# Optimization experiments

Hardware: AMD Instinct MI355X
Metric: run time of the kernel (lower is better)

## Reference

```python
import jax, jax.numpy as jnp
import numpy as np

N = 50000
E = 800000
NUM_GRAPHS = 128
X_IN, HID, EDGE_DIM = 64, 64, 16


def setup_inputs() -> dict:
    key = jax.random.key(0)
    ks = jax.random.split(key, 9)
    s = 0.05
    inp = {
        'x': jax.random.normal(ks[0], (N, X_IN), jnp.float32),
        'edge_index': jax.random.randint(ks[1], (2, E), 0, N, dtype=jnp.int32),
        'edge_attr': jax.random.normal(ks[2], (E, EDGE_DIM), jnp.float32),
        'batch': jnp.sort(jax.random.randint(ks[3], (N,), 0, NUM_GRAPHS, dtype=jnp.int32)),
        'w_fc1': jax.random.normal(ks[4], (EDGE_DIM, 1), jnp.float32) * s,
        'b_fc1': jnp.zeros((1,), jnp.float32),
    }
    dims = [(X_IN, HID), (HID, HID * 2), (HID * 2, HID)]
    for i, (din, dout) in enumerate(dims):
        k1, k2, k3 = jax.random.split(ks[5 + i], 3)
        inp[f'w1_{i}'] = jax.random.normal(k1, (din, dout), jnp.float32) * s
        inp[f'b1_{i}'] = jnp.zeros((dout,), jnp.float32)
        inp[f'w2_{i}'] = jax.random.normal(k2, (din, dout), jnp.float32) * s
        inp[f'w3_{i}'] = jax.random.normal(k3, (din, dout), jnp.float32) * s
        inp[f'b3_{i}'] = jnp.zeros((dout,), jnp.float32)
    return inp


def leconv(x, src, dst, ew, w1, b1, w2, w3, b3):
    # PyG LEConv: out_i = lin3(x_i) + sum_{j->i} e_ji * (lin1(x_j) - lin2(x_i))
    a = x @ w1 + b1          # lin1 (bias=True)   [N, out]
    b = x @ w2               # lin2 (bias=False)  [N, out]
    msg = ew[:, None] * (a[src] - b[dst])          # [E, out]
    agg = jax.ops.segment_sum(msg, dst, num_segments=N)
    return agg + x @ w3 + b3  # lin3 (bias=True)


def reference(x, edge_index, edge_attr, batch,
              w_fc1, b_fc1,
              w1_0, b1_0, w2_0, w3_0, b3_0,
              w1_1, b1_1, w2_1, w3_1, b3_1,
              w1_2, b1_2, w2_2, w3_2, b3_2):
    src, dst = edge_index[0], edge_index[1]
    ew = (edge_attr @ w_fc1 + b_fc1)[:, 0]         # fc1(edge_attr).squeeze(-1) -> [E]
    h = jax.nn.elu(leconv(x, src, dst, ew, w1_0, b1_0, w2_0, w3_0, b3_0))
    h = jax.nn.elu(leconv(h, src, dst, ew, w1_1, b1_1, w2_1, w3_1, b3_1))
    h = jax.nn.elu(leconv(h, src, dst, ew, w1_2, b1_2, w2_2, w3_2, b3_2))
    # global max pool over nodes of each graph -> [NUM_GRAPHS, HID]
    return jax.ops.segment_max(h, batch, num_segments=NUM_GRAPHS)
```

## Files before the change

### kernel.cpp

```cpp
#include <hip/hip_runtime.h>
#include <math.h>

#define N_NODES 50000
#define N_EDGES 800000
#define NUM_GRAPHS_ 128
#define SCAN_NB 98
#define NPASS 8
#define NODES_PER_PASS 6250
#define HCHUNKS 128
#define EDGES_PER_CHUNK 6250
#define HWORDS 12500

typedef unsigned short u16;
typedef unsigned int u32;
typedef __attribute__((ext_vector_type(8))) short bf16x8;
typedef __attribute__((ext_vector_type(4))) float f32x4;

__device__ __forceinline__ float elu_f(float v) {
    return v > 0.f ? v : (__expf(v) - 1.f);
}
__device__ __forceinline__ u16 f2bf(float f) {
    u32 u = __float_as_uint(f);
    u += 0x7FFFu + ((u >> 16) & 1u);
    return (u16)(u >> 16);
}
__device__ __forceinline__ float bf2f(u16 h) {
    return __uint_as_float(((u32)h) << 16);
}
__device__ __forceinline__ void bfpair(u32 v, float& lo, float& hi) {
    lo = __uint_as_float(v << 16);
    hi = __uint_as_float(v & 0xFFFF0000u);
}
__device__ __forceinline__ u32 packbf(float lo, float hi) {
    return (u32)f2bf(lo) | ((u32)f2bf(hi) << 16);
}

__global__ void conv_x_kernel(const float* __restrict__ x, u16* __restrict__ xb) {
    int g = blockIdx.x * blockDim.x + threadIdx.x;
    float4 v = ((const float4*)x)[g];
    uint2 o;
    o.x = packbf(v.x, v.y);
    o.y = packbf(v.z, v.w);
    ((uint2*)xb)[g] = o;
}

__global__ void ew_kernel(const float* __restrict__ edge_attr,
                          const float* __restrict__ w_fc1,
                          const float* __restrict__ b_fc1,
                          const int* __restrict__ edge_index,
                          float* __restrict__ ew,
                          u16* __restrict__ dst16) {
    int e = blockIdx.x * blockDim.x + threadIdx.x;
    if (e >= N_EDGES) return;
    const float4* ea = (const float4*)(edge_attr + (size_t)e * 16);
    const float4* wf = (const float4*)w_fc1;
    float acc = b_fc1[0];
#pragma unroll
    for (int i = 0; i < 4; i++) {
        float4 a = ea[i], w = wf[i];
        acc += a.x * w.x + a.y * w.y + a.z * w.z + a.w * w.w;
    }
    ew[e] = acc;
    dst16[e] = (u16)edge_index[N_EDGES + e];
}

__global__ __launch_bounds__(256) void deg_hist_kernel(const u16* __restrict__ dst16,
                                                       u32* __restrict__ partial) {
    __shared__ u32 bins[HWORDS];
    const int c = blockIdx.x >> 1;
    const int p = blockIdx.x & 1;
    const int t = threadIdx.x;
    for (int i = t; i < HWORDS; i += 256) bins[i] = 0;
    __syncthreads();
    const int base = c * EDGES_PER_CHUNK;
    const int nlo = p * 25000;
    for (int i = t; i < EDGES_PER_CHUNK; i += 256) {
        const int b = (int)dst16[base + i] - nlo;
        if ((unsigned)b < 25000u)
            atomicAdd(&bins[b >> 1], 1u << ((b & 1) * 16));
    }
    __syncthreads();
    u32* outp = partial + (size_t)blockIdx.x * HWORDS;
    for (int i = t; i < HWORDS; i += 256) outp[i] = bins[i];
}

__global__ __launch_bounds__(256) void scan_chunks_kernel(const u32* __restrict__ partial,
                                                          u32* __restrict__ prefpack,
                                                          u32* __restrict__ degpack) {
    const int g = blockIdx.x * 256 + threadIdx.x;
    if (g >= 25000) return;
    const int p = (g >= HWORDS) ? 1 : 0;
    const int wh = g - p * HWORDS;
    u32 runlo = 0, runhi = 0;
    for (int c = 0; c < HCHUNKS; c++) {
        prefpack[(size_t)c * 25000 + g] = runlo | (runhi << 16);
        u32 v = partial[(size_t)((c << 1) + p) * HWORDS + wh];
        runlo += v & 0xFFFFu;
        runhi += v >> 16;
    }
    degpack[g] = runlo | (runhi << 16);
}

__global__ __launch_bounds__(256) void scan1_kernel(const u32* __restrict__ degpack,
                                                    int* __restrict__ rowptr,
                                                    int* __restrict__ blk_sums) {
    __shared__ int sh[256];
    const int t = threadIdx.x;
    const int base = blockIdx.x * 512;
    const int i0 = base + 2 * t, i1 = i0 + 1;
    int d0 = 0, d1 = 0;
    if (i0 < N_NODES) {
        u32 v = degpack[i0 >> 1];
        d0 = (int)(v & 0xFFFFu);
        d1 = (int)(v >> 16);
    }
    const int pair = d0 + d1;
    int v = pair;
    sh[t] = v;
    __syncthreads();
#pragma unroll
    for (int off = 1; off < 256; off <<= 1) {
        int add = (t >= off) ? sh[t - off] : 0;
        __syncthreads();
        v += add;
        sh[t] = v;
        __syncthreads();
    }
    const int excl = v - pair;
    if (i0 < N_NODES) rowptr[i0] = excl;
    if (i1 < N_NODES) rowptr[i1] = excl + d0;
    if (t == 255) blk_sums[blockIdx.x] = v;
}

__global__ __launch_bounds__(128) void scan2_kernel(const int* __restrict__ blk_sums,
                                                    int* __restrict__ blk_offs,
                                                    int* __restrict__ rowptr) {
    __shared__ int sh[128];
    const int t = threadIdx.x;
    const int orig = (t < SCAN_NB) ? blk_sums[t] : 0;
    int v = orig;
    sh[t] = v;
    __syncthreads();
#pragma unroll
    for (int off = 1; off < 128; off <<= 1) {
        int add = (t >= off) ? sh[t - off] : 0;
        __syncthreads();
        v += add;
        sh[t] = v;
        __syncthreads();
    }
    if (t < SCAN_NB) blk_offs[t] = v - orig;
    if (t == 127) rowptr[N_NODES] = v;
}

__global__ void scan3_kernel(int* __restrict__ rowptr,
                             const int* __restrict__ blk_offs) {
    int i = blockIdx.x * blockDim.x + threadIdx.x;
    if (i >= N_NODES) return;
    rowptr[i] += blk_offs[i >> 9];
}

__global__ __launch_bounds__(256) void place_kernel(const int* __restrict__ edge_index,
                                                    const float* __restrict__ ew,
                                                    const u16* __restrict__ dst16,
                                                    const int* __restrict__ rowptr,
                                                    const u32* __restrict__ prefpack,
                                                    int2* __restrict__ csr) {
    __shared__ int lcur[NODES_PER_PASS];
    const int pass = blockIdx.x & (NPASS - 1);
    const int c = blockIdx.x >> 3;
    const int lo = pass * NODES_PER_PASS;
    const int t = threadIdx.x;
    for (int i = t; i < NODES_PER_PASS; i += 256) lcur[i] = 0;
    __syncthreads();
    const int base = c * EDGES_PER_CHUNK;
    for (int i = t; i < EDGES_PER_CHUNK; i += 256) {
        const int e = base + i;
        const int d = (int)dst16[e];
        const int dl = d - lo;
        if ((unsigned)dl < (unsigned)NODES_PER_PASS) {
            u32 pw = prefpack[(size_t)c * 25000 + (d >> 1)];
            int pref = (int)((pw >> ((d & 1) * 16)) & 0xFFFFu);
            int lpos = atomicAdd(&lcur[dl], 1);
            int2 ent;
            ent.x = edge_index[e];
            ent.y = __float_as_int(ew[e]);
            csr[rowptr[d] + pref + lpos] = ent;
        }
    }
}

template <int DIN, bool WRITE_C>
__global__ __launch_bounds__(256) void gather_kernel(
    const u16* __restrict__ xb, const int* __restrict__ rowptr,
    const int2* __restrict__ csr, u16* __restrict__ sb,
    u16* __restrict__ chb, float* __restrict__ c) {
    constexpr int CG = DIN / 4;
    constexpr int EG = 64 / CG;
    const int gid = blockIdx.x * 256 + threadIdx.x;
    const int node = gid >> 6;
    if (node >= N_NODES) return;
    const int lane = threadIdx.x & 63;
    const int cg = lane & (CG - 1);
    const int eg = lane / CG;
    const int beg = rowptr[node];
    const int end = rowptr[node + 1];
    const uint2* x2 = (const uint2*)xb;

    float a0 = 0.f, a1 = 0.f, a2 = 0.f, a3 = 0.f;
    float b0 = 0.f, b1 = 0.f, b2 = 0.f, b3 = 0.f;
    float wsum = 0.f;

    int p = beg + eg;
    for (; p + EG < end; p += 2 * EG) {
        int2 e0 = csr[p];
        int2 e1 = csr[p + EG];
        float w0 = __int_as_float(e0.y);
        float w1 = __int_as_float(e1.y);
        uint2 v0 = x2[(size_t)e0.x * CG + cg];
        uint2 v1 = x2[(size_t)e1.x * CG + cg];
        float f0, f1, f2, f3, g0, g1, g2, g3;
        bfpair(v0.x, f0, f1); bfpair(v0.y, f2, f3);
        bfpair(v1.x, g0, g1); bfpair(v1.y, g2, g3);
        a0 += w0 * f0; a1 += w0 * f1; a2 += w0 * f2; a3 += w0 * f3;
        b0 += w1 * g0; b1 += w1 * g1; b2 += w1 * g2; b3 += w1 * g3;
        wsum += w0 + w1;
    }
    if (p < end) {
        int2 e0 = csr[p];
        float w0 = __int_as_float(e0.y);
        uint2 v0 = x2[(size_t)e0.x * CG + cg];
        float f0, f1, f2, f3;
        bfpair(v0.x, f0, f1); bfpair(v0.y, f2, f3);
        a0 += w0 * f0; a1 += w0 * f1; a2 += w0 * f2; a3 += w0 * f3;
        wsum += w0;
    }
    a0 += b0; a1 += b1; a2 += b2; a3 += b3;

#pragma unroll
    for (int off = 32; off >= CG; off >>= 1) {
        a0 += __shfl_xor(a0, off);
        a1 += __shfl_xor(a1, off);
        a2 += __shfl_xor(a2, off);
        a3 += __shfl_xor(a3, off);
        wsum += __shfl_xor(wsum, off);
    }

    if (lane < CG) {
        uint2 so;
        so.x = packbf(a0, a1);
        so.y = packbf(a2, a3);
        ((uint2*)sb)[(size_t)node * CG + cg] = so;
        const float cn = WRITE_C ? wsum : c[node];
        uint2 hv = x2[(size_t)node * CG + cg];
        float h0, h1, h2, h3;
        bfpair(hv.x, h0, h1); bfpair(hv.y, h2, h3);
        uint2 co;
        co.x = packbf(cn * h0, cn * h1);
        co.y = packbf(cn * h2, cn * h3);
        ((uint2*)chb)[(size_t)node * CG + cg] = co;
    }
    if (WRITE_C && lane == 0) c[node] = wsum;
}

__global__ void pack_w_kernel(const float* __restrict__ w3_0, const float* __restrict__ w1_0, const float* __restrict__ w2_0,
                              const float* __restrict__ w3_1, const float* __restrict__ w1_1, const float* __restrict__ w2_1,
                              const float* __restrict__ w3_2, const float* __restrict__ w1_2, const float* __restrict__ w2_2,
                              u16* __restrict__ bp0, u16* __restrict__ bp1, u16* __restrict__ bp2) {
    int t = blockIdx.x * blockDim.x + threadIdx.x;
    if (t >= 7680) return;
    u16 buf[8];
    if (t < 4608) {
        int DIN, DOUT, lid;
        const float *w3, *w1, *w2;
        u16* bp;
        if (t < 1536) { DIN = 64; DOUT = 64;  lid = t;        w3 = w3_0; w1 = w1_0; w2 = w2_0; bp = bp0; }
        else          { DIN = 64; DOUT = 128; lid = t - 1536; w3 = w3_1; w1 = w1_1; w2 = w2_1; bp = bp1; }
        const int NT = DOUT / 16;
        const int lane = lid & 63;
        const int fragid = lid >> 6;
        const int chunk = fragid / NT;
        const int ntile = fragid % NT;
        const int n = ntile * 16 + (lane & 15);
        const int kbase = chunk * 32 + (lane >> 4) * 8;
#pragma unroll
        for (int j = 0; j < 8; j++) {
            int k = kbase + j;
            int region = k / DIN;
            int kk = k - region * DIN;
            float v = (region == 0) ? w3[kk * DOUT + n]
                    : (region == 1) ? w1[kk * DOUT + n]
                                    : -w2[kk * DOUT + n];
            buf[j] = f2bf(v);
        }
        *(bf16x8*)(bp + ((size_t)lid << 3)) = *(bf16x8*)buf;
    } else {
        const int lid = t - 4608;
        const int NT = 12;
        const int lane = lid & 63;
        const int fragid = lid >> 6;
        const int chunk = fragid / NT;
        const int ntile = fragid % NT;
        const int n = ntile * 16 + (lane & 15);
        const int kbase = chunk * 32 + (lane >> 4) * 8;
#pragma unroll
        for (int j = 0; j < 8; j++) {
            int k = kbase + j;
            float v = (n < 64)  ? w3_2[k * 64 + n]
                    : (n < 128) ? -w2_2[k * 64 + (n - 64)]
                                : w1_2[k * 64 + (n - 128)];
            buf[j] = f2bf(v);
        }
        *(bf16x8*)(bp2 + ((size_t)lid << 3)) = *(bf16x8*)buf;
    }
}

template <int DIN, int DOUT>
__global__ __launch_bounds__(256) void gemm_mfma(
    const u16* __restrict__ hb, const u16* __restrict__ sb,
    const u16* __restrict__ chb, const u16* __restrict__ Bp,
    const float* __restrict__ cvec, const float* __restrict__ bias1,
    const float* __restrict__ bias3, u16* __restrict__ outp) {
    constexpr int CH = DIN / 32;
    constexpr int CHUNKS = 3 * CH;
    constexpr int NT = DOUT / 16;
    const int tid = threadIdx.x;
    const int wv = tid >> 6;
    const int lane = tid & 63;
    const int l15 = lane & 15;
    const int q = lane >> 4;
    const int mhalf = wv & 1;
    const int nhalf = wv >> 1;
    const int row_base = blockIdx.x * 64 + mhalf * 32;
    const int nt0 = blockIdx.y * 4 + nhalf * 2;

    const int r0 = min(row_base + l15, N_NODES - 1);
    const int r1 = min(row_base + 16 + l15, N_NODES - 1);
    const int qo = q * 8;

    f32x4 acc00 = {0.f, 0.f, 0.f, 0.f};
    f32x4 acc01 = {0.f, 0.f, 0.f, 0.f};
    f32x4 acc10 = {0.f, 0.f, 0.f, 0.f};
    f32x4 acc11 = {0.f, 0.f, 0.f, 0.f};

#pragma unroll
    for (int chunk = 0; chunk < CHUNKS; chunk++) {
        const int region = chunk / CH;
        const int koff = (chunk - region * CH) * 32 + qo;
        const u16* A = (region == 0) ? hb : (region == 1) ? sb : chb;
        bf16x8 a0 = *(const bf16x8*)(A + (size_t)r0 * DIN + koff);
        bf16x8 a1 = *(const bf16x8*)(A + (size_t)r1 * DIN + koff);
        const u16* bp = Bp + (((size_t)(chunk * NT + nt0) * 64 + lane) << 3);
        bf16x8 bf0 = *(const bf16x8*)bp;
        bf16x8 bf1 = *(const bf16x8*)(bp + 64 * 8);
        acc00 = __builtin_amdgcn_mfma_f32_16x16x32_bf16(a0, bf0, acc00, 0, 0, 0);
        acc01 = __builtin_amdgcn_mfma_f32_16x16x32_bf16(a0, bf1, acc01, 0, 0, 0);
        acc10 = __builtin_amdgcn_mfma_f32_16x16x32_bf16(a1, bf0, acc10, 0, 0, 0);
        acc11 = __builtin_amdgcn_mfma_f32_16x16x32_bf16(a1, bf1, acc11, 0, 0, 0);
    }

#pragma unroll
    for (int ni = 0; ni < 2; ni++) {
        const int col = (nt0 + ni) * 16 + l15;
        const float B3 = bias3[col];
        const float B1 = bias1[col];
        const f32x4 am0 = ni ? acc01 : acc00;
        const f32x4 am1 = ni ? acc11 : acc10;
#pragma unroll
        for (int mi = 0; mi < 2; mi++) {
            const f32x4 av = mi ? am1 : am0;
#pragma unroll
            for (int reg = 0; reg < 4; reg++) {
                const int row = row_base + mi * 16 + q * 4 + reg;
                if (row < N_NODES) {
                    const float cv = cvec[row];
                    const float val = av[reg] + B3 + cv * B1;
                    outp[(size_t)row * DOUT + col] = f2bf(elu_f(val));
                }
            }
        }
    }
}

__global__ __launch_bounds__(256) void gemm_l1_fused(
    const u16* __restrict__ hb, const u16* __restrict__ sb,
    const u16* __restrict__ chb, const u16* __restrict__ Bp1,
    const u16* __restrict__ Bp2, const float* __restrict__ cvec,
    const float* __restrict__ bias1, const float* __restrict__ bias3,
    u16* __restrict__ zuy) {
    __shared__ u16 ht[64][136];
    const int tid = threadIdx.x;
    const int wv = tid >> 6;
    const int lane = tid & 63;
    const int l15 = lane & 15;
    const int q = lane >> 4;
    const int mhalf = wv & 1;
    const int nhalf = wv >> 1;
    const int row_base = blockIdx.x * 64 + mhalf * 32;
    const int r0 = min(row_base + l15, N_NODES - 1);
    const int r1 = min(row_base + 16 + l15, N_NODES - 1);
    const int qo = q * 8;

    {
        const int nt0 = nhalf * 4;
        f32x4 acc[2][4] = {};
#pragma unroll
        for (int chunk = 0; chunk < 6; chunk++) {
            const int region = chunk / 2;
            const int koff = (chunk - region * 2) * 32 + qo;
            const u16* A = (region == 0) ? hb : (region == 1) ? sb : chb;
            bf16x8 a0 = *(const bf16x8*)(A + (size_t)r0 * 64 + koff);
            bf16x8 a1 = *(const bf16x8*)(A + (size_t)r1 * 64 + koff);
#pragma unroll
            for (int ni = 0; ni < 4; ni++) {
                bf16x8 bf = *(const bf16x8*)(Bp1 + (((size_t)(chunk * 8 + nt0 + ni) * 64 + lane) << 3));
                acc[0][ni] = __builtin_amdgcn_mfma_f32_16x16x32_bf16(a0, bf, acc[0][ni], 0, 0, 0);
                acc[1][ni] = __builtin_amdgcn_mfma_f32_16x16x32_bf16(a1, bf, acc[1][ni], 0, 0, 0);
            }
        }
#pragma unroll
        for (int ni = 0; ni < 4; ni++) {
            const int col = (nt0 + ni) * 16 + l15;
            const float B3 = bias3[col];
            const float B1 = bias1[col];
#pragma unroll
            for (int mi = 0; mi < 2; mi++) {
#pragma unroll
                for (int reg = 0; reg < 4; reg++) {
                    const int lrow = mhalf * 32 + mi * 16 + q * 4 + reg;
                    const int grow = blockIdx.x * 64 + lrow;
                    const float cv = cvec[min(grow, N_NODES - 1)];
                    ht[lrow][col] = f2bf(elu_f(acc[mi][ni][reg] + B3 + cv * B1));
                }
            }
        }
    }
    __syncthreads();

    {
        const int nt2 = nhalf * 6;
        f32x4 acc[2][6] = {};
#pragma unroll
        for (int chunk = 0; chunk < 4; chunk++) {
            const int koff = chunk * 32 + qo;
            bf16x8 a0 = *(const bf16x8*)(&ht[mhalf * 32 + l15][koff]);
            bf16x8 a1 = *(const bf16x8*)(&ht[mhalf * 32 + 16 + l15][koff]);
#pragma unroll
            for (int ni = 0; ni < 6; ni++) {
                bf16x8 bf = *(const bf16x8*)(Bp2 + (((size_t)(chunk * 12 + nt2 + ni) * 64 + lane) << 3));
                acc[0][ni] = __builtin_amdgcn_mfma_f32_16x16x32_bf16(a0, bf, acc[0][ni], 0, 0, 0);
                acc[1][ni] = __builtin_amdgcn_mfma_f32_16x16x32_bf16(a1, bf, acc[1][ni], 0, 0, 0);
            }
        }
#pragma unroll
        for (int ni = 0; ni < 6; ni++) {
            const int col = (nt2 + ni) * 16 + l15;
#pragma unroll
            for (int mi = 0; mi < 2; mi++) {
#pragma unroll
                for (int reg = 0; reg < 4; reg++) {
                    const int row = row_base + mi * 16 + q * 4 + reg;
                    if (row < N_NODES)
                        zuy[(size_t)row * 192 + col] = f2bf(acc[mi][ni][reg]);
                }
            }
        }
    }
}

__global__ __launch_bounds__(256) void gather2_kernel(
    const u16* __restrict__ zuy, const int* __restrict__ rowptr,
    const int2* __restrict__ csr, const float* __restrict__ c,
    const float* __restrict__ bias1, const float* __restrict__ bias3,
    u16* __restrict__ h3) {
    constexpr int CG = 16, EG = 4;
    const int gid = blockIdx.x * 256 + threadIdx.x;
    const int node = gid >> 6;
    if (node >= N_NODES) return;
    const int lane = threadIdx.x & 63;
    const int cg = lane & (CG - 1);
    const int eg = lane >> 4;
    const int beg = rowptr[node];
    const int end = rowptr[node + 1];

    float a0 = 0.f, a1 = 0.f, a2 = 0.f, a3 = 0.f;
    float b0 = 0.f, b1 = 0.f, b2 = 0.f, b3 = 0.f;

    int p = beg + eg;
    for (; p + EG < end; p += 2 * EG) {
        int2 e0 = csr[p];
        int2 e1 = csr[p + EG];
        float w0 = __int_as_float(e0.y);
        float w1 = __int_as_float(e1.y);
        uint2 v0 = ((const uint2*)(zuy + (size_t)e0.x * 192 + 128))[cg];
        uint2 v1 = ((const uint2*)(zuy + (size_t)e1.x * 192 + 128))[cg];
        float f0, f1, f2, f3, g0, g1, g2, g3;
        bfpair(v0.x, f0, f1); bfpair(v0.y, f2, f3);
        bfpair(v1.x, g0, g1); bfpair(v1.y, g2, g3);
        a0 += w0 * f0; a1 += w0 * f1; a2 += w0 * f2; a3 += w0 * f3;
        b0 += w1 * g0; b1 += w1 * g1; b2 += w1 * g2; b3 += w1 * g3;
    }
    if (p < end) {
        int2 e0 = csr[p];
        float w0 = __int_as_float(e0.y);
        uint2 v0 = ((const uint2*)(zuy + (size_t)e0.x * 192 + 128))[cg];
        float f0, f1, f2, f3;
        bfpair(v0.x, f0, f1); bfpair(v0.y, f2, f3);
        a0 += w0 * f0; a1 += w0 * f1; a2 += w0 * f2; a3 += w0 * f3;
    }
    a0 += b0; a1 += b1; a2 += b2; a3 += b3;

#pragma unroll
    for (int off = 32; off >= CG; off >>= 1) {
        a0 += __shfl_xor(a0, off);
        a1 += __shfl_xor(a1, off);
        a2 += __shfl_xor(a2, off);
        a3 += __shfl_xor(a3, off);
    }

    if (lane < CG) {
        const float cn = c[node];
        const u16* zr = zuy + (size_t)node * 192;
        uint2 zv = ((const uint2*)zr)[cg];
        uint2 uv = ((const uint2*)(zr + 64))[cg];
        float z0, z1, z2, z3, u0, u1, u2, u3;
        bfpair(zv.x, z0, z1); bfpair(zv.y, z2, z3);
        bfpair(uv.x, u0, u1); bfpair(uv.y, u2, u3);
        const float4 b3v = *(const float4*)(bias3 + cg * 4);
        const float4 b1v = *(const float4*)(bias1 + cg * 4);
        float o0 = elu_f(z0 + cn * u0 + a0 + b3v.x + cn * b1v.x);
        float o1 = elu_f(z1 + cn * u1 + a1 + b3v.y + cn * b1v.y);
        float o2 = elu_f(z2 + cn * u2 + a2 + b3v.z + cn * b1v.z);
        float o3 = elu_f(z3 + cn * u3 + a3 + b3v.w + cn * b1v.w);
        uint2 o;
        o.x = packbf(o0, o1);
        o.y = packbf(o2, o3);
        ((uint2*)h3)[(size_t)node * CG + cg] = o;
    }
}

__global__ void pool_kernel(const u16* __restrict__ h,
                            const int* __restrict__ batch,
                            float* __restrict__ out) {
    const int g = blockIdx.x;
    const int tid = threadIdx.x;
    int lo = 0, hi = N_NODES;
    while (lo < hi) { int mid = (lo + hi) >> 1; if (batch[mid] < g) lo = mid + 1; else hi = mid; }
    const int beg = lo;
    lo = beg; hi = N_NODES;
    while (lo < hi) { int mid = (lo + hi) >> 1; if (batch[mid] < g + 1) lo = mid + 1; else hi = mid; }
    const int end = lo;

    __shared__ float red[256];
    const int col = tid & 63;
    const int rg = tid >> 6;
    float m = -3.0e38f;
    for (int r = beg + rg; r < end; r += 4) m = fmaxf(m, bf2f(h[(size_t)r * 64 + col]));
    red[tid] = m;
    __syncthreads();
    if (tid < 64) {
        m = fmaxf(fmaxf(red[tid], red[tid + 64]), fmaxf(red[tid + 128], red[tid + 192]));
        out[g * 64 + tid] = m;
    }
}

extern "C" void kernel_launch(void* const* d_in, const int* in_sizes, int n_in,
                              void* d_out, int out_size, void* d_ws, size_t ws_size,
                              hipStream_t stream) {
    const float* x = (const float*)d_in[0];
    const int* ei = (const int*)d_in[1];
    const float* ea = (const float*)d_in[2];
    const int* batch = (const int*)d_in[3];
    const float* wfc = (const float*)d_in[4];
    const float* bfc = (const float*)d_in[5];
    const float* w1_0 = (const float*)d_in[6];
    const float* b1_0 = (const float*)d_in[7];
    const float* w2_0 = (const float*)d_in[8];
    const float* w3_0 = (const float*)d_in[9];
    const float* b3_0 = (const float*)d_in[10];
    const float* w1_1 = (const float*)d_in[11];
    const float* b1_1 = (const float*)d_in[12];
    const float* w2_1 = (const float*)d_in[13];
    const float* w3_1 = (const float*)d_in[14];
    const float* b3_1 = (const float*)d_in[15];
    const float* w1_2 = (const float*)d_in[16];
    const float* b1_2 = (const float*)d_in[17];
    const float* w2_2 = (const float*)d_in[18];
    const float* w3_2 = (const float*)d_in[19];
    const float* b3_2 = (const float*)d_in[20];
    float* out = (float*)d_out;

    char* ws = (char*)d_ws;
    float* ew      = (float*)(ws);
    float* c       = (float*)(ws + 3200000);
    int*   rowptr  = (int*)  (ws + 3800000);
    int2*  csr     = (int2*) (ws + 4000128);
    u16*   xb      = (u16*)  (ws + 10400128);
    u16*   sb      = (u16*)  (ws + 16800128);
    u16*   chb     = (u16*)  (ws + 29600128);
    u16*   h1      = (u16*)  (ws + 42400128);
    u16*   zuy     = (u16*)  (ws + 48800128);
    u16*   bp0     = (u16*)  (ws + 68000128);
    u16*   bp1     = (u16*)  (ws + 68024704);
    u16*   bp2     = (u16*)  (ws + 68073856);
    int* blk_sums  = (int*)  (ws + 68123008);
    int* blk_offs  = (int*)  (ws + 68123520);
    u16* dst16   = chb;
    u32* degpack = (u32*)(ws + 31600128);
    u32* partial = (u32*)sb;
    u32* prefpack = (u32*)zuy;
    u16* h3 = xb;

    conv_x_kernel<<<3125, 256, 0, stream>>>(x, xb);
    ew_kernel<<<(N_EDGES + 255) / 256, 256, 0, stream>>>(ea, wfc, bfc, ei, ew, dst16);
    pack_w_kernel<<<30, 256, 0, stream>>>(w3_0, w1_0, w2_0, w3_1, w1_1, w2_1,
                                          w3_2, w1_2, w2_2, bp0, bp1, bp2);
    deg_hist_kernel<<<HCHUNKS * 2, 256, 0, stream>>>(dst16, partial);
    scan_chunks_kernel<<<98, 256, 0, stream>>>(partial, prefpack, degpack);
    scan1_kernel<<<SCAN_NB, 256, 0, stream>>>(degpack, rowptr, blk_sums);
    scan2_kernel<<<1, 128, 0, stream>>>(blk_sums, blk_offs, rowptr);
    scan3_kernel<<<(N_NODES + 255) / 256, 256, 0, stream>>>(rowptr, blk_offs);
    place_kernel<<<HCHUNKS * NPASS, 256, 0, stream>>>(ei, ew, dst16, rowptr, prefpack, csr);

    const int RB = (N_NODES + 63) / 64;
    const int GBLK = (N_NODES * 64 + 255) / 256;

    gather_kernel<64, true><<<GBLK, 256, 0, stream>>>(xb, rowptr, csr, sb, chb, c);
    gemm_mfma<64, 64><<<dim3(RB, 1), 256, 0, stream>>>(xb, sb, chb, bp0, c, b1_0, b3_0, h1);

    gather_kernel<64, false><<<GBLK, 256, 0, stream>>>(h1, rowptr, csr, sb, chb, c);
    gemm_l1_fused<<<RB, 256, 0, stream>>>(h1, sb, chb, bp1, bp2, c, b1_1, b3_1, zuy);

    gather2_kernel<<<GBLK, 256, 0, stream>>>(zuy, rowptr, csr, c, b1_2, b3_2, h3);

    pool_kernel<<<NUM_GRAPHS_, 256, 0, stream>>>(h3, batch, out);
}
```

Baseline: 337.5 us.

## Fuse prep kernels and parallelize chunk prefix scan across chunk quarters

Result: faster. 329.2 us (-2.4%).

```diff
diff --git a/kernel.cpp b/kernel.cpp
--- a/kernel.cpp
+++ b/kernel.cpp
@@ -10,6 +10,7 @@
 #define HCHUNKS 128
 #define EDGES_PER_CHUNK 6250
 #define HWORDS 12500
+#define TS_BPH 196
 
 typedef unsigned short u16;
 typedef unsigned int u32;
@@ -35,33 +36,84 @@
     return (u32)f2bf(lo) | ((u32)f2bf(hi) << 16);
 }
 
-__global__ void conv_x_kernel(const float* __restrict__ x, u16* __restrict__ xb) {
-    int g = blockIdx.x * blockDim.x + threadIdx.x;
-    float4 v = ((const float4*)x)[g];
-    uint2 o;
-    o.x = packbf(v.x, v.y);
-    o.y = packbf(v.z, v.w);
-    ((uint2*)xb)[g] = o;
-}
-
-__global__ void ew_kernel(const float* __restrict__ edge_attr,
-                          const float* __restrict__ w_fc1,
-                          const float* __restrict__ b_fc1,
-                          const int* __restrict__ edge_index,
-                          float* __restrict__ ew,
-                          u16* __restrict__ dst16) {
-    int e = blockIdx.x * blockDim.x + threadIdx.x;
-    if (e >= N_EDGES) return;
-    const float4* ea = (const float4*)(edge_attr + (size_t)e * 16);
-    const float4* wf = (const float4*)w_fc1;
-    float acc = b_fc1[0];
-#pragma unroll
-    for (int i = 0; i < 4; i++) {
-        float4 a = ea[i], w = wf[i];
-        acc += a.x * w.x + a.y * w.y + a.z * w.z + a.w * w.w;
-    }
-    ew[e] = acc;
-    dst16[e] = (u16)edge_index[N_EDGES + e];
+__global__ void prep_kernel(const float* __restrict__ edge_attr,
+                            const float* __restrict__ w_fc1,
+                            const float* __restrict__ b_fc1,
+                            const int* __restrict__ edge_index,
+                            float* __restrict__ ew,
+                            u16* __restrict__ dst16,
+                            const float* __restrict__ x, u16* __restrict__ xb,
+                            const float* __restrict__ w3_0, const float* __restrict__ w1_0, const float* __restrict__ w2_0,
+                            const float* __restrict__ w3_1, const float* __restrict__ w1_1, const float* __restrict__ w2_1,
+                            const float* __restrict__ w3_2, const float* __restrict__ w1_2, const float* __restrict__ w2_2,
+                            u16* __restrict__ bp0, u16* __restrict__ bp1, u16* __restrict__ bp2) {
+    const int b = blockIdx.x;
+    if (b < 3125) {
+        const int e = b * 256 + threadIdx.x;
+        const float4* ea = (const float4*)(edge_attr + (size_t)e * 16);
+        const float4* wf = (const float4*)w_fc1;
+        float acc = b_fc1[0];
+#pragma unroll
+        for (int i = 0; i < 4; i++) {
+            float4 a = ea[i], w = wf[i];
+            acc += a.x * w.x + a.y * w.y + a.z * w.z + a.w * w.w;
+        }
+        ew[e] = acc;
+        dst16[e] = (u16)edge_index[N_EDGES + e];
+    } else if (b < 6250) {
+        const int g = (b - 3125) * 256 + threadIdx.x;
+        float4 v = ((const float4*)x)[g];
+        uint2 o;
+        o.x = packbf(v.x, v.y);
+        o.y = packbf(v.z, v.w);
+        ((uint2*)xb)[g] = o;
+    } else {
+        const int t = (b - 6250) * 256 + threadIdx.x;
+        u16 buf[8];
+        if (t < 4608) {
+            int DOUT, lid;
+            const float *w3, *w1, *w2;
+            u16* bp;
+            if (t < 1536) { DOUT = 64;  lid = t;        w3 = w3_0; w1 = w1_0; w2 = w2_0; bp = bp0; }
+            else          { DOUT = 128; lid = t - 1536; w3 = w3_1; w1 = w1_1; w2 = w2_1; bp = bp1; }
+            const int NT = DOUT / 16;
+            const int lane = lid & 63;
+            const int fragid = lid >> 6;
+            const int chunk = fragid / NT;
+            const int ntile = fragid % NT;
+            const int n = ntile * 16 + (lane & 15);
+            const int kbase = chunk * 32 + (lane >> 4) * 8;
+#pragma unroll
+            for (int j = 0; j < 8; j++) {
+                int k = kbase + j;
+                int region = k / 64;
+                int kk = k - region * 64;
+                float v = (region == 0) ? w3[kk * DOUT + n]
+                        : (region == 1) ? w1[kk * DOUT + n]
+                                        : -w2[kk * DOUT + n];
+                buf[j] = f2bf(v);
+            }
+            *(bf16x8*)(bp + ((size_t)lid << 3)) = *(bf16x8*)buf;
+        } else if (t < 7680) {
+            const int lid = t - 4608;
+            const int NT = 12;
+            const int lane = lid & 63;
+            const int fragid = lid >> 6;
+            const int chunk = fragid / NT;
+            const int ntile = fragid % NT;
+            const int n = ntile * 16 + (lane & 15);
+            const int kbase = chunk * 32 + (lane >> 4) * 8;
+#pragma unroll
+            for (int j = 0; j < 8; j++) {
+                int k = kbase + j;
+                float v = (n < 64)  ? w3_2[k * 64 + n]
+                        : (n < 128) ? -w2_2[k * 64 + (n - 64)]
+                                    : w1_2[k * 64 + (n - 128)];
+                buf[j] = f2bf(v);
+            }
+            *(bf16x8*)(bp2 + ((size_t)lid << 3)) = *(bf16x8*)buf;
+        }
+    }
 }
 
 __global__ __launch_bounds__(256) void deg_hist_kernel(const u16* __restrict__ dst16,
@@ -87,18 +139,41 @@
 __global__ __launch_bounds__(256) void scan_chunks_kernel(const u32* __restrict__ partial,
                                                           u32* __restrict__ prefpack,
                                                           u32* __restrict__ degpack) {
-    const int g = blockIdx.x * 256 + threadIdx.x;
-    if (g >= 25000) return;
-    const int p = (g >= HWORDS) ? 1 : 0;
-    const int wh = g - p * HWORDS;
-    u32 runlo = 0, runhi = 0;
-    for (int c = 0; c < HCHUNKS; c++) {
-        prefpack[(size_t)c * 25000 + g] = runlo | (runhi << 16);
-        u32 v = partial[(size_t)((c << 1) + p) * HWORDS + wh];
-        runlo += v & 0xFFFFu;
-        runhi += v >> 16;
-    }
-    degpack[g] = runlo | (runhi << 16);
+    __shared__ u32 qsums[4][64];
+    const int t = threadIdx.x;
+    const int p = (blockIdx.x >= TS_BPH) ? 1 : 0;
+    const int wh0 = (blockIdx.x - p * TS_BPH) << 6;
+    const int wl = t & 63;
+    const int cq = t >> 6;
+    const int wh = wh0 + wl;
+    const bool ok = wh < HWORDS;
+
+    u32 vals[32];
+#pragma unroll
+    for (int i = 0; i < 32; i++) {
+        const int c = cq * 32 + i;
+        vals[i] = ok ? partial[(size_t)((c << 1) + p) * HWORDS + wh] : 0u;
+    }
+    u32 s = 0;
+#pragma unroll
+    for (int i = 0; i < 32; i++) s += vals[i];
+    qsums[cq][wl] = s;
+    __syncthreads();
+    u32 run = 0;
+#pragma unroll
+    for (int j = 0; j < 4; j++)
+        if (j < cq) run += qsums[j][wl];
+
+    if (ok) {
+        const int g = p * HWORDS + wh;
+#pragma unroll
+        for (int i = 0; i < 32; i++) {
+            const int c = cq * 32 + i;
+            prefpack[(size_t)c * 25000 + g] = run;
+            run += vals[i];
+        }
+        if (cq == 3) degpack[g] = run;
+    }
 }
 
 __global__ __launch_bounds__(256) void scan1_kernel(const u32* __restrict__ degpack,
@@ -261,58 +336,6 @@
         ((uint2*)chb)[(size_t)node * CG + cg] = co;
     }
     if (WRITE_C && lane == 0) c[node] = wsum;
-}
-
-__global__ void pack_w_kernel(const float* __restrict__ w3_0, const float* __restrict__ w1_0, const float* __restrict__ w2_0,
-                              const float* __restrict__ w3_1, const float* __restrict__ w1_1, const float* __restrict__ w2_1,
-                              const float* __restrict__ w3_2, const float* __restrict__ w1_2, const float* __restrict__ w2_2,
-                              u16* __restrict__ bp0, u16* __restrict__ bp1, u16* __restrict__ bp2) {
-    int t = blockIdx.x * blockDim.x + threadIdx.x;
-    if (t >= 7680) return;
-    u16 buf[8];
-    if (t < 4608) {
-        int DIN, DOUT, lid;
-        const float *w3, *w1, *w2;
-        u16* bp;
-        if (t < 1536) { DIN = 64; DOUT = 64;  lid = t;        w3 = w3_0; w1 = w1_0; w2 = w2_0; bp = bp0; }
-        else          { DIN = 64; DOUT = 128; lid = t - 1536; w3 = w3_1; w1 = w1_1; w2 = w2_1; bp = bp1; }
-        const int NT = DOUT / 16;
-        const int lane = lid & 63;
-        const int fragid = lid >> 6;
-        const int chunk = fragid / NT;
-        const int ntile = fragid % NT;
-        const int n = ntile * 16 + (lane & 15);
-        const int kbase = chunk * 32 + (lane >> 4) * 8;
-#pragma unroll
-        for (int j = 0; j < 8; j++) {
-            int k = kbase + j;
-            int region = k / DIN;
-            int kk = k - region * DIN;
-            float v = (region == 0) ? w3[kk * DOUT + n]
-                    : (region == 1) ? w1[kk * DOUT + n]
-                                    : -w2[kk * DOUT + n];
-            buf[j] = f2bf(v);
-        }
-        *(bf16x8*)(bp + ((size_t)lid << 3)) = *(bf16x8*)buf;
-    } else {
-        const int lid = t - 4608;
-        const int NT = 12;
-        const int lane = lid & 63;
-        const int fragid = lid >> 6;
-        const int chunk = fragid / NT;
-        const int ntile = fragid % NT;
-        const int n = ntile * 16 + (lane & 15);
-        const int kbase = chunk * 32 + (lane >> 4) * 8;
-#pragma unroll
-        for (int j = 0; j < 8; j++) {
-            int k = kbase + j;
-            float v = (n < 64)  ? w3_2[k * 64 + n]
-                    : (n < 128) ? -w2_2[k * 64 + (n - 64)]
-                                : w1_2[k * 64 + (n - 128)];
-            buf[j] = f2bf(v);
-        }
-        *(bf16x8*)(bp2 + ((size_t)lid << 3)) = *(bf16x8*)buf;
-    }
 }
 
 template <int DIN, int DOUT>
@@ -611,12 +634,11 @@
     u32* prefpack = (u32*)zuy;
     u16* h3 = xb;
 
-    conv_x_kernel<<<3125, 256, 0, stream>>>(x, xb);
-    ew_kernel<<<(N_EDGES + 255) / 256, 256, 0, stream>>>(ea, wfc, bfc, ei, ew, dst16);
-    pack_w_kernel<<<30, 256, 0, stream>>>(w3_0, w1_0, w2_0, w3_1, w1_1, w2_1,
+    prep_kernel<<<6280, 256, 0, stream>>>(ea, wfc, bfc, ei, ew, dst16, x, xb,
+                                          w3_0, w1_0, w2_0, w3_1, w1_1, w2_1,
                                           w3_2, w1_2, w2_2, bp0, bp1, bp2);
     deg_hist_kernel<<<HCHUNKS * 2, 256, 0, stream>>>(dst16, partial);
-    scan_chunks_kernel<<<98, 256, 0, stream>>>(partial, prefpack, degpack);
+    scan_chunks_kernel<<<TS_BPH * 2, 256, 0, stream>>>(partial, prefpack, degpack);
     scan1_kernel<<<SCAN_NB, 256, 0, stream>>>(degpack, rowptr, blk_sums);
     scan2_kernel<<<1, 128, 0, stream>>>(blk_sums, blk_offs, rowptr);
     scan3_kernel<<<(N_NODES + 255) / 256, 256, 0, stream>>>(rowptr, blk_offs);
```
